# Performance work log

Hardware: AMD Instinct MI355X
Metric: run time of the kernel (lower is better)

## Reference

```python
import jax, jax.numpy as jnp
import numpy as np

C_Z = 128
N_HEADS = 4
HEAD_DIM = 32
TOTAL = N_HEADS * HEAD_DIM
B, N = 1, 256


def setup_inputs() -> dict:
    key = jax.random.key(0)
    ks = jax.random.split(key, 10)
    s = lambda k, sh: jax.random.normal(k, sh, dtype=jnp.float32) * 0.02
    return {
        "pair_representation": jax.random.normal(ks[0], (B, N, N, C_Z), dtype=jnp.float32),
        "ln_gamma": jnp.ones((C_Z,), jnp.float32),
        "ln_beta": jnp.zeros((C_Z,), jnp.float32),
        "Wq": s(ks[1], (C_Z, TOTAL)),
        "Wk": s(ks[2], (C_Z, TOTAL)),
        "Wv": s(ks[3], (C_Z, TOTAL)),
        "Wb": s(ks[4], (C_Z, N_HEADS)),
        "Wg": s(ks[5], (C_Z, TOTAL)),
        "bg": jnp.zeros((TOTAL,), jnp.float32),
        "Wo": s(ks[6], (TOTAL, C_Z)),
        "bo": jnp.zeros((C_Z,), jnp.float32),
    }


def reference(pair_representation, ln_gamma, ln_beta, Wq, Wk, Wv, Wb, Wg, bg, Wo, bo):
    x = pair_representation
    # LayerNorm over c_z
    mu = jnp.mean(x, axis=-1, keepdims=True)
    var = jnp.mean((x - mu) ** 2, axis=-1, keepdims=True)
    x = (x - mu) * jax.lax.rsqrt(var + 1e-5) * ln_gamma + ln_beta

    b, n, _, _ = x.shape
    split = lambda t: t.reshape(b, n, n, N_HEADS, HEAD_DIM)
    Q = split(x @ Wq)  # [b,i,j,h,d]
    K = split(x @ Wk)
    V = split(x @ Wv)
    G = jax.nn.sigmoid(split(x @ Wg + bg))
    Bias = x @ Wb  # [b,j,k,h]

    scores = jnp.einsum("bijhd,bikhd->bijkh", Q, K) / np.float32(np.sqrt(HEAD_DIM))
    scores = scores + Bias[:, None]  # broadcast over i
    attn = jax.nn.softmax(scores, axis=3)  # over k
    vals = jnp.einsum("bijkh,bikhd->bijhd", attn, V)
    vals = (G * vals).reshape(b, n, n, TOTAL)
    return vals @ Wo + bo
```

## Files before the change

### kernel.cpp

```cpp
#include <hip/hip_runtime.h>
#include <hip/hip_bf16.h>


#define QSCALE 0.17677669529663687f

typedef __attribute__((ext_vector_type(8))) short bf16x8;
typedef __attribute__((ext_vector_type(4))) short bf16x4;
typedef __attribute__((ext_vector_type(4))) float f32x4;

#define MFMA32(a, b, c) __builtin_amdgcn_mfma_f32_16x16x32_bf16((a), (b), (c), 0, 0, 0)

__device__ __forceinline__ f32x4 mfma16_asm(bf16x4 a, bf16x4 b, f32x4 c) {
    f32x4 d;
    asm volatile("v_mfma_f32_16x16x16_bf16 %0, %1, %2, %3"
                 : "=v"(d) : "v"(a), "v"(b), "v"(c));
    return d;
}

#if !defined(__HIP_DEVICE_COMPILE__)
#define MFMA16(a, b, c) (c)
#elif __has_builtin(__builtin_amdgcn_mfma_f32_16x16x16bf16_1k)
#define MFMA16(a, b, c) __builtin_amdgcn_mfma_f32_16x16x16bf16_1k((a), (b), (c), 0, 0, 0)
#else
#define MFMA16(a, b, c) mfma16_asm((a), (b), (c))
#endif

__device__ __forceinline__ ushort f2bf(float f) {
    uint32_t u = __builtin_bit_cast(uint32_t, f);
    uint32_t r = (u + 0x7FFFu + ((u >> 16) & 1u)) >> 16;
    return (ushort)r;
}
__device__ __forceinline__ uint pk2(float a, float b) {
    union { __hip_bfloat162 h; uint u; } cv;
    cv.h = __float22bfloat162_rn(make_float2(a, b));
    return cv.u;
}

__global__ __launch_bounds__(256) void prep_bias_kernel(
    const float* __restrict__ Wq, const float* __restrict__ Wk, const float* __restrict__ Wv,
    const float* __restrict__ Wg, const float* __restrict__ Wo, const float* __restrict__ Wb,
    const float* __restrict__ x, const float* __restrict__ gamma, const float* __restrict__ beta,
    ushort* __restrict__ Wfrag, ushort* __restrict__ WoFrag,
    ushort* __restrict__ xn, float* __restrict__ BbF)
{
    __shared__ float WbS[512];
    __shared__ float gS[128];
    __shared__ float bS[128];

    if (blockIdx.x < 320) {
        int idx = blockIdx.x * 256 + threadIdx.x;
        if (idx < 65536) {
            int j = idx & 7, lane = (idx >> 3) & 63, ks = (idx >> 9) & 3, ct = idx >> 11;
            int n = ct * 16 + (lane & 15);
            int k = ks * 32 + (lane >> 4) * 8 + j;
            float v;
            if (n < 128)      v = Wq[k * 128 + n] * QSCALE;
            else if (n < 256) v = Wk[k * 128 + (n - 128)];
            else if (n < 384) v = Wv[k * 128 + (n - 256)];
            else              v = Wg[k * 128 + (n - 384)];
            Wfrag[idx] = f2bf(v);
        } else {
            int idx2 = idx - 65536;
            int j = idx2 & 7, lane = (idx2 >> 3) & 63, ks = (idx2 >> 9) & 3, ct = idx2 >> 11;
            int n = ct * 16 + (lane & 15);
            int k = ks * 32 + (lane >> 4) * 8 + j;
            WoFrag[idx2] = f2bf(Wo[k * 128 + n]);
        }
        return;
    }

    const int t = threadIdx.x;
    if (t < 128)      { *(f32x4*)&WbS[t * 4] = *(const f32x4*)(Wb + t * 4); }
    else if (t < 160) { int c = (t - 128) * 4; *(f32x4*)&gS[c] = *(const f32x4*)(gamma + c); }
    else if (t < 192) { int c = (t - 160) * 4; *(f32x4*)&bS[c] = *(const f32x4*)(beta + c); }
    __syncthreads();

    const int wave = t >> 6, lane = t & 63, m = lane & 15, quad = lane >> 4;
    const int p = (blockIdx.x - 320) * 64 + wave * 16 + m;

    const float* rp0 = x + (size_t)p * 128;
    f32x4 xa[4][2];
    float sum = 0.f, ssq = 0.f;
#pragma unroll
    for (int ks = 0; ks < 4; ++ks) {
        xa[ks][0] = *(const f32x4*)(rp0 + ks * 32 + quad * 8);
        xa[ks][1] = *(const f32x4*)(rp0 + ks * 32 + quad * 8 + 4);
#pragma unroll
        for (int q4 = 0; q4 < 2; ++q4) {
            f32x4 v = xa[ks][q4];
            sum += v[0] + v[1] + v[2] + v[3];
            ssq += v[0]*v[0] + v[1]*v[1] + v[2]*v[2] + v[3]*v[3];
        }
    }
    sum += __shfl_xor(sum, 16); ssq += __shfl_xor(ssq, 16);
    sum += __shfl_xor(sum, 32); ssq += __shfl_xor(ssq, 32);
    const float mu   = sum * (1.f / 128.f);
    const float rstd = rsqrtf(ssq * (1.f / 128.f) - mu * mu + 1e-5f);

    float b0 = 0.f, b1 = 0.f, b2 = 0.f, b3 = 0.f;
#pragma unroll
    for (int ks = 0; ks < 4; ++ks) {
        uint4 pkd;
        uint pw[4];
#pragma unroll
        for (int q4 = 0; q4 < 2; ++q4) {
            const int c = ks * 32 + quad * 8 + q4 * 4;
            f32x4 v = xa[ks][q4];
            float n0 = (v[0] - mu) * rstd * gS[c + 0] + bS[c + 0];
            float n1 = (v[1] - mu) * rstd * gS[c + 1] + bS[c + 1];
            float n2 = (v[2] - mu) * rstd * gS[c + 2] + bS[c + 2];
            float n3 = (v[3] - mu) * rstd * gS[c + 3] + bS[c + 3];
            pw[q4 * 2]     = pk2(n0, n1);
            pw[q4 * 2 + 1] = pk2(n2, n3);
            f32x4 w0 = *(const f32x4*)&WbS[(c + 0) * 4];
            f32x4 w1 = *(const f32x4*)&WbS[(c + 1) * 4];
            f32x4 w2 = *(const f32x4*)&WbS[(c + 2) * 4];
            f32x4 w3 = *(const f32x4*)&WbS[(c + 3) * 4];
            b0 += n0*w0[0] + n1*w1[0] + n2*w2[0] + n3*w3[0];
            b1 += n0*w0[1] + n1*w1[1] + n2*w2[1] + n3*w3[1];
            b2 += n0*w0[2] + n1*w1[2] + n2*w2[2] + n3*w3[2];
            b3 += n0*w0[3] + n1*w1[3] + n2*w2[3] + n3*w3[3];
        }
        pkd.x = pw[0]; pkd.y = pw[1]; pkd.z = pw[2]; pkd.w = pw[3];
        *(uint4*)(xn + (size_t)p * 128 + ks * 32 + quad * 8) = pkd;
    }
    b0 += __shfl_xor(b0, 16); b1 += __shfl_xor(b1, 16); b2 += __shfl_xor(b2, 16); b3 += __shfl_xor(b3, 16);
    b0 += __shfl_xor(b0, 32); b1 += __shfl_xor(b1, 32); b2 += __shfl_xor(b2, 32); b3 += __shfl_xor(b3, 32);

    if (quad == 0) {
        const int row = p >> 8, col = p & 255;
        float bb[4] = {b0, b1, b2, b3};
#pragma unroll
        for (int r = 0; r < 4; ++r) {
            int addr = (((r * 16 + (row >> 4)) * 16 + (col >> 4)) * 64 +
                        ((col & 15) >> 2) * 16 + (row & 15)) * 4 + (col & 3);
            BbF[addr] = bb[r];
        }
    }
}

__global__ __launch_bounds__(256, 4) void fused_kernel(
    const ushort* __restrict__ xn, const ushort* __restrict__ Wfrag,
    const float* __restrict__ bg, const float* __restrict__ BbF,
    ushort* __restrict__ gvals)
{
    __shared__ __align__(16) ushort SM[18688];
    ushort* QK = SM;
    ushort* VT = SM + 10240;

    const int t = threadIdx.x;
    const int w = t >> 6, lane = t & 63, m = lane & 15, quad = lane >> 4;
    const int i = blockIdx.x >> 2, h = blockIdx.x & 3;
    const ushort* xb = xn + ((size_t)i << 15);

    {
        const ushort* Wm = Wfrag + (0 + h * 2) * 2048;
        bf16x8 wfr[2][4];
#pragma unroll
        for (int ctl = 0; ctl < 2; ++ctl)
#pragma unroll
            for (int ks = 0; ks < 4; ++ks)
                wfr[ctl][ks] = *(const bf16x8*)(Wm + ctl * 2048 + ks * 512 + lane * 8);
#pragma unroll
        for (int grp = 0; grp < 4; ++grp) {
            const int j = w * 64 + grp * 16 + m;
            bf16x8 xg[4];
            const ushort* xp = xb + (size_t)j * 128 + quad * 8;
#pragma unroll
            for (int ks = 0; ks < 4; ++ks) xg[ks] = *(const bf16x8*)(xp + ks * 32);
#pragma unroll
            for (int ctl = 0; ctl < 2; ++ctl) {
                f32x4 acc = (f32x4){0.f, 0.f, 0.f, 0.f};
#pragma unroll
                for (int ks = 0; ks < 4; ++ks) acc = MFMA32(wfr[ctl][ks], xg[ks], acc);
                uint2 u; u.x = pk2(acc[0], acc[1]); u.y = pk2(acc[2], acc[3]);
                *(uint2*)(QK + j * 40 + ctl * 16 + quad * 4) = u;
            }
        }
    }
    bf16x8 qf[4];
#pragma unroll
    for (int jt = 0; jt < 4; ++jt)
        qf[jt] = *(const bf16x8*)(QK + (w * 64 + jt * 16 + m) * 40 + quad * 8);
    asm volatile("" ::: "memory");

    {
        const ushort* Wm = Wfrag + (8 + h * 2) * 2048;
        bf16x8 wfr[2][4];
#pragma unroll
        for (int ctl = 0; ctl < 2; ++ctl)
#pragma unroll
            for (int ks = 0; ks < 4; ++ks)
                wfr[ctl][ks] = *(const bf16x8*)(Wm + ctl * 2048 + ks * 512 + lane * 8);
#pragma unroll
        for (int grp = 0; grp < 4; ++grp) {
            const int k = w * 64 + grp * 16 + m;
            bf16x8 xg[4];
            const ushort* xp = xb + (size_t)k * 128 + quad * 8;
#pragma unroll
            for (int ks = 0; ks < 4; ++ks) xg[ks] = *(const bf16x8*)(xp + ks * 32);
#pragma unroll
            for (int ctl = 0; ctl < 2; ++ctl) {
                f32x4 acc = (f32x4){0.f, 0.f, 0.f, 0.f};
#pragma unroll
                for (int ks = 0; ks < 4; ++ks) acc = MFMA32(wfr[ctl][ks], xg[ks], acc);
                uint2 u; u.x = pk2(acc[0], acc[1]); u.y = pk2(acc[2], acc[3]);
                *(uint2*)(QK + k * 40 + ctl * 16 + quad * 4) = u;
            }
        }
    }
    asm volatile("" ::: "memory");

    {
        const ushort* Wm = Wfrag + (16 + h * 2) * 2048;
        bf16x8 wfr[2][4];
#pragma unroll
        for (int ctl = 0; ctl < 2; ++ctl)
#pragma unroll
            for (int ks = 0; ks < 4; ++ks)
                wfr[ctl][ks] = *(const bf16x8*)(Wm + ctl * 2048 + ks * 512 + lane * 8);
#pragma unroll
        for (int grp = 0; grp < 4; ++grp) {
            const int k = w * 64 + grp * 16 + m;
            bf16x8 xg[4];
            const ushort* xp = xb + (size_t)k * 128 + quad * 8;
#pragma unroll
            for (int ks = 0; ks < 4; ++ks) xg[ks] = *(const bf16x8*)(xp + ks * 32);
#pragma unroll
            for (int ctl = 0; ctl < 2; ++ctl) {
                f32x4 acc = (f32x4){0.f, 0.f, 0.f, 0.f};
#pragma unroll
                for (int ks = 0; ks < 4; ++ks) acc = MFMA32(wfr[ctl][ks], xg[ks], acc);
#pragma unroll
                for (int r = 0; r < 4; ++r)
                    VT[(ctl * 16 + quad * 4 + r) * 264 + k] = f2bf(acc[r]);
            }
        }
    }
    __syncthreads();

    f32x4 O[4][2];
    float lsum[4];
#pragma unroll
    for (int jt = 0; jt < 4; ++jt) {
        O[jt][0] = (f32x4){0.f, 0.f, 0.f, 0.f};
        O[jt][1] = (f32x4){0.f, 0.f, 0.f, 0.f};
        lsum[jt] = 0.f;
    }
    const float* bb = BbF + ((size_t)(h * 16 + w * 4) << 12) + (lane << 2);

    for (int kh = 0; kh < 16; ++kh) {
        bf16x8 kf = *(const bf16x8*)(QK + (kh * 16 + m) * 40 + quad * 8);
        bf16x4 vf[2];
#pragma unroll
        for (int dt = 0; dt < 2; ++dt) {
            uint2 vv = *(const uint2*)(VT + (dt * 16 + m) * 264 + kh * 16 + quad * 4);
            vf[dt] = __builtin_bit_cast(bf16x4, vv);
        }
#pragma unroll
        for (int jt = 0; jt < 4; ++jt) {
            f32x4 S = *(const f32x4*)(bb + (jt << 12) + (kh << 8));
            S = MFMA32(kf, qf[jt], S);
            float p0 = __expf(S[0]), p1 = __expf(S[1]);
            float p2 = __expf(S[2]), p3 = __expf(S[3]);
            lsum[jt] += p0 + p1 + p2 + p3;
            uint2 pu; pu.x = pk2(p0, p1); pu.y = pk2(p2, p3);
            bf16x4 pf = __builtin_bit_cast(bf16x4, pu);
#pragma unroll
            for (int dt = 0; dt < 2; ++dt)
                O[jt][dt] = MFMA16(vf[dt], pf, O[jt][dt]);
        }
    }

#pragma unroll
    for (int jt = 0; jt < 4; ++jt) {
        float s = lsum[jt];
        s += __shfl_xor(s, 16);
        s += __shfl_xor(s, 32);
        lsum[jt] = 1.f / s;
    }

    {
        const ushort* Wm = Wfrag + (24 + h * 2) * 2048;
        bf16x8 wfr[2][4];
        f32x4 bg4[2];
#pragma unroll
        for (int ctl = 0; ctl < 2; ++ctl) {
#pragma unroll
            for (int ks = 0; ks < 4; ++ks)
                wfr[ctl][ks] = *(const bf16x8*)(Wm + ctl * 2048 + ks * 512 + lane * 8);
            bg4[ctl] = *(const f32x4*)(bg + h * 32 + ctl * 16 + quad * 4);
        }
#pragma unroll
        for (int grp = 0; grp < 4; ++grp) {
            const int j = w * 64 + grp * 16 + m;
            const float rl = lsum[grp];
            bf16x8 xg[4];
            const ushort* xp = xb + (size_t)j * 128 + quad * 8;
#pragma unroll
            for (int ks = 0; ks < 4; ++ks) xg[ks] = *(const bf16x8*)(xp + ks * 32);
#pragma unroll
            for (int ctl = 0; ctl < 2; ++ctl) {
                f32x4 acc = (f32x4){0.f, 0.f, 0.f, 0.f};
#pragma unroll
                for (int ks = 0; ks < 4; ++ks) acc = MFMA32(wfr[ctl][ks], xg[ks], acc);
                float g0 = 1.f / (1.f + __expf(-(acc[0] + bg4[ctl][0])));
                float g1 = 1.f / (1.f + __expf(-(acc[1] + bg4[ctl][1])));
                float g2 = 1.f / (1.f + __expf(-(acc[2] + bg4[ctl][2])));
                float g3 = 1.f / (1.f + __expf(-(acc[3] + bg4[ctl][3])));
                float v0 = O[grp][ctl][0] * rl * g0;
                float v1 = O[grp][ctl][1] * rl * g1;
                float v2 = O[grp][ctl][2] * rl * g2;
                float v3 = O[grp][ctl][3] * rl * g3;
                uint2 u; u.x = pk2(v0, v1); u.y = pk2(v2, v3);
                *(uint2*)(gvals + (size_t)(i * 256 + j) * 128 + h * 32 + ctl * 16 + quad * 4) = u;
            }
        }
    }
}

__global__ __launch_bounds__(256) void oproj_kernel(
    const ushort* __restrict__ gvals, const ushort* __restrict__ WoFrag,
    const float* __restrict__ bo, float* __restrict__ out)
{
    __shared__ ushort Bs[8 * 2048];
    const int t = threadIdx.x;
    const int wave = t >> 6, lane = t & 63, m = lane & 15, quad = lane >> 4;
    const int p0 = blockIdx.x * 64;
    {
        const uint4* src = (const uint4*)WoFrag;
        uint4* dst = (uint4*)Bs;
#pragma unroll
        for (int r = 0; r < 8; ++r) dst[r * 256 + t] = src[r * 256 + t];
    }
    bf16x8 gf[4];
    const int p = p0 + wave * 16 + m;
#pragma unroll
    for (int ks = 0; ks < 4; ++ks)
        gf[ks] = *(const bf16x8*)(gvals + (size_t)p * 128 + ks * 32 + quad * 8);
    __syncthreads();

#pragma unroll
    for (int ct = 0; ct < 8; ++ct) {
        f32x4 acc = (f32x4){0.f, 0.f, 0.f, 0.f};
#pragma unroll
        for (int ks = 0; ks < 4; ++ks) {
            bf16x8 wfr = ((const bf16x8*)Bs)[(ct * 4 + ks) * 64 + lane];
            acc = MFMA32(wfr, gf[ks], acc);
        }
        const int c0 = ct * 16 + quad * 4;
        f32x4 bov = *(const f32x4*)(bo + c0);
        float4 v = make_float4(acc[0] + bov[0], acc[1] + bov[1],
                               acc[2] + bov[2], acc[3] + bov[3]);
        *(float4*)(&out[(size_t)p * 128 + c0]) = v;
    }
}

extern "C" void kernel_launch(void* const* d_in, const int* in_sizes, int n_in,
                              void* d_out, int out_size, void* d_ws, size_t ws_size,
                              hipStream_t stream) {
    const float* x     = (const float*)d_in[0];
    const float* gamma = (const float*)d_in[1];
    const float* beta  = (const float*)d_in[2];
    const float* Wq    = (const float*)d_in[3];
    const float* Wk    = (const float*)d_in[4];
    const float* Wv    = (const float*)d_in[5];
    const float* Wb    = (const float*)d_in[6];
    const float* Wg    = (const float*)d_in[7];
    const float* bg    = (const float*)d_in[8];
    const float* Wo    = (const float*)d_in[9];
    const float* bo    = (const float*)d_in[10];

    ushort* ws      = (ushort*)d_ws;
    ushort* Wfrag   = ws;
    ushort* WoFragp = ws + 65536;
    ushort* xn      = ws + 81920;
    ushort* gvals   = ws + 81920 + 8388608;
    float*  BbF     = (float*)(ws + 81920 + 2 * 8388608);

    prep_bias_kernel<<<1344, 256, 0, stream>>>(Wq, Wk, Wv, Wg, Wo, Wb,
                                               x, gamma, beta,
                                               Wfrag, WoFragp, xn, BbF);
    fused_kernel<<<1024, 256, 0, stream>>>(xn, Wfrag, bg, BbF, gvals);
    oproj_kernel<<<1024, 256, 0, stream>>>(gvals, WoFragp, bo, (float*)d_out);
}
```

Before: 172.6 us.

## Fuse output projection into attention kernel with one block per row

Merges the separate output-projection kernel into the attention kernel. Each 512-thread block now covers one row i across all four heads, so the gated values are staged in shared memory and multiplied by Wo in place, with no global round trip. The pair bias is also pre-exponentiated in the prep kernel, turning the in-loop bias add into a multiply of exp(S). Shared memory layouts are XOR-swizzled to avoid bank conflicts. In exchange the kernel uses 128KB of dynamic shared memory with one block per CU and only 256 blocks, which cuts occupancy and the parallelism available to hide latency.

Result: faster. 162.5 us (-5.9%).

```diff
diff --git a/kernel.cpp b/kernel.cpp
--- a/kernel.cpp
+++ b/kernel.cpp
@@ -41,7 +41,7 @@
     const float* __restrict__ Wg, const float* __restrict__ Wo, const float* __restrict__ Wb,
     const float* __restrict__ x, const float* __restrict__ gamma, const float* __restrict__ beta,
     ushort* __restrict__ Wfrag, ushort* __restrict__ WoFrag,
-    ushort* __restrict__ xn, float* __restrict__ BbF)
+    ushort* __restrict__ xn, float* __restrict__ EbF)
 {
     __shared__ float WbS[512];
     __shared__ float gS[128];
@@ -134,27 +134,32 @@
         for (int r = 0; r < 4; ++r) {
             int addr = (((r * 16 + (row >> 4)) * 16 + (col >> 4)) * 64 +
                         ((col & 15) >> 2) * 16 + (row & 15)) * 4 + (col & 3);
-            BbF[addr] = bb[r];
-        }
-    }
-}
-
-__global__ __launch_bounds__(256, 4) void fused_kernel(
+            EbF[addr] = __expf(bb[r]);
+        }
+    }
+}
+
+__global__ __launch_bounds__(512, 1) void fused_kernel(
     const ushort* __restrict__ xn, const ushort* __restrict__ Wfrag,
-    const float* __restrict__ bg, const float* __restrict__ BbF,
-    ushort* __restrict__ gvals)
+    const float* __restrict__ bg, const float* __restrict__ EbF,
+    const ushort* __restrict__ WoFrag, const float* __restrict__ bo,
+    float* __restrict__ out)
 {
-    __shared__ __align__(16) ushort SM[18688];
-    ushort* QK = SM;
-    ushort* VT = SM + 10240;
+    extern __shared__ __align__(16) ushort SM[];
+    ushort* KL = SM;
+    ushort* VT = SM + 32768;
+
+    const f32x4 ZERO4 = {0.f, 0.f, 0.f, 0.f};
 
     const int t = threadIdx.x;
     const int w = t >> 6, lane = t & 63, m = lane & 15, quad = lane >> 4;
-    const int i = blockIdx.x >> 2, h = blockIdx.x & 3;
+    const int i = blockIdx.x;
+    const int h = w >> 1, half = w & 1;
+    const int jbase = half * 128;
     const ushort* xb = xn + ((size_t)i << 15);
 
     {
-        const ushort* Wm = Wfrag + (0 + h * 2) * 2048;
+        const ushort* Wm = Wfrag + (h * 2) * 2048;
         bf16x8 wfr[2][4];
 #pragma unroll
         for (int ctl = 0; ctl < 2; ++ctl)
@@ -162,26 +167,31 @@
             for (int ks = 0; ks < 4; ++ks)
                 wfr[ctl][ks] = *(const bf16x8*)(Wm + ctl * 2048 + ks * 512 + lane * 8);
 #pragma unroll
-        for (int grp = 0; grp < 4; ++grp) {
-            const int j = w * 64 + grp * 16 + m;
+        for (int grp = 0; grp < 8; ++grp) {
+            const int jloc = grp * 16 + m;
             bf16x8 xg[4];
-            const ushort* xp = xb + (size_t)j * 128 + quad * 8;
+            const ushort* xp = xb + (size_t)(jbase + jloc) * 128 + quad * 8;
 #pragma unroll
             for (int ks = 0; ks < 4; ++ks) xg[ks] = *(const bf16x8*)(xp + ks * 32);
 #pragma unroll
             for (int ctl = 0; ctl < 2; ++ctl) {
-                f32x4 acc = (f32x4){0.f, 0.f, 0.f, 0.f};
+                f32x4 acc = ZERO4;
 #pragma unroll
                 for (int ks = 0; ks < 4; ++ks) acc = MFMA32(wfr[ctl][ks], xg[ks], acc);
+                const int c = ctl * 16 + quad * 4;
+                const int idx = (w * 4096 + jloc * 32 + c) ^ ((jloc & 3) << 3);
                 uint2 u; u.x = pk2(acc[0], acc[1]); u.y = pk2(acc[2], acc[3]);
-                *(uint2*)(QK + j * 40 + ctl * 16 + quad * 4) = u;
+                *(uint2*)(KL + idx) = u;
             }
         }
     }
-    bf16x8 qf[4];
-#pragma unroll
-    for (int jt = 0; jt < 4; ++jt)
-        qf[jt] = *(const bf16x8*)(QK + (w * 64 + jt * 16 + m) * 40 + quad * 8);
+    bf16x8 qf[8];
+#pragma unroll
+    for (int jt = 0; jt < 8; ++jt) {
+        const int jloc = jt * 16 + m;
+        const int idx = (w * 4096 + jloc * 32 + quad * 8) ^ ((jloc & 3) << 3);
+        qf[jt] = *(const bf16x8*)(KL + idx);
+    }
     asm volatile("" ::: "memory");
 
     {
@@ -193,23 +203,24 @@
             for (int ks = 0; ks < 4; ++ks)
                 wfr[ctl][ks] = *(const bf16x8*)(Wm + ctl * 2048 + ks * 512 + lane * 8);
 #pragma unroll
-        for (int grp = 0; grp < 4; ++grp) {
-            const int k = w * 64 + grp * 16 + m;
+        for (int grp = 0; grp < 8; ++grp) {
+            const int k = jbase + grp * 16 + m;
             bf16x8 xg[4];
             const ushort* xp = xb + (size_t)k * 128 + quad * 8;
 #pragma unroll
             for (int ks = 0; ks < 4; ++ks) xg[ks] = *(const bf16x8*)(xp + ks * 32);
 #pragma unroll
             for (int ctl = 0; ctl < 2; ++ctl) {
-                f32x4 acc = (f32x4){0.f, 0.f, 0.f, 0.f};
+                f32x4 acc = ZERO4;
 #pragma unroll
                 for (int ks = 0; ks < 4; ++ks) acc = MFMA32(wfr[ctl][ks], xg[ks], acc);
+                const int d0 = ctl * 16 + quad * 4;
+                const int idx = (h * 8192 + (k >> 1) * 64 + (k & 1) * 32 + d0) ^ (((k >> 1) & 7) << 3);
                 uint2 u; u.x = pk2(acc[0], acc[1]); u.y = pk2(acc[2], acc[3]);
-                *(uint2*)(QK + k * 40 + ctl * 16 + quad * 4) = u;
+                *(uint2*)(KL + idx) = u;
             }
         }
     }
-    asm volatile("" ::: "memory");
 
     {
         const ushort* Wm = Wfrag + (16 + h * 2) * 2048;
@@ -220,49 +231,61 @@
             for (int ks = 0; ks < 4; ++ks)
                 wfr[ctl][ks] = *(const bf16x8*)(Wm + ctl * 2048 + ks * 512 + lane * 8);
 #pragma unroll
-        for (int grp = 0; grp < 4; ++grp) {
-            const int k = w * 64 + grp * 16 + m;
+        for (int grp = 0; grp < 8; ++grp) {
+            const int k = jbase + grp * 16 + m;
             bf16x8 xg[4];
             const ushort* xp = xb + (size_t)k * 128 + quad * 8;
 #pragma unroll
             for (int ks = 0; ks < 4; ++ks) xg[ks] = *(const bf16x8*)(xp + ks * 32);
 #pragma unroll
             for (int ctl = 0; ctl < 2; ++ctl) {
-                f32x4 acc = (f32x4){0.f, 0.f, 0.f, 0.f};
+                f32x4 acc = ZERO4;
 #pragma unroll
                 for (int ks = 0; ks < 4; ++ks) acc = MFMA32(wfr[ctl][ks], xg[ks], acc);
 #pragma unroll
-                for (int r = 0; r < 4; ++r)
-                    VT[(ctl * 16 + quad * 4 + r) * 264 + k] = f2bf(acc[r]);
+                for (int r = 0; r < 4; ++r) {
+                    const int d = ctl * 16 + quad * 4 + r;
+                    const int idx = ((h * 32 + d) * 256 + k) ^ ((d & 7) << 3);
+                    VT[idx] = f2bf(acc[r]);
+                }
             }
         }
     }
     __syncthreads();
 
-    f32x4 O[4][2];
-    float lsum[4];
-#pragma unroll
-    for (int jt = 0; jt < 4; ++jt) {
-        O[jt][0] = (f32x4){0.f, 0.f, 0.f, 0.f};
-        O[jt][1] = (f32x4){0.f, 0.f, 0.f, 0.f};
+    f32x4 O[8][2];
+    float lsum[8];
+#pragma unroll
+    for (int jt = 0; jt < 8; ++jt) {
+        O[jt][0] = ZERO4;
+        O[jt][1] = ZERO4;
         lsum[jt] = 0.f;
     }
-    const float* bb = BbF + ((size_t)(h * 16 + w * 4) << 12) + (lane << 2);
+    const float* ebB = EbF + ((size_t)(h * 16 + half * 8) << 12) + (lane << 2);
 
     for (int kh = 0; kh < 16; ++kh) {
-        bf16x8 kf = *(const bf16x8*)(QK + (kh * 16 + m) * 40 + quad * 8);
+        f32x4 eb[8];
+#pragma unroll
+        for (int jt = 0; jt < 8; ++jt)
+            eb[jt] = *(const f32x4*)(ebB + (jt << 12) + (kh << 8));
+        const int k = kh * 16 + m;
+        const int kidx = (h * 8192 + (k >> 1) * 64 + (k & 1) * 32 + quad * 8) ^ (((k >> 1) & 7) << 3);
+        bf16x8 kf = *(const bf16x8*)(KL + kidx);
         bf16x4 vf[2];
 #pragma unroll
         for (int dt = 0; dt < 2; ++dt) {
-            uint2 vv = *(const uint2*)(VT + (dt * 16 + m) * 264 + kh * 16 + quad * 4);
+            const int d = dt * 16 + m;
+            const int vidx = ((h * 32 + d) * 256 + kh * 16 + quad * 4) ^ ((d & 7) << 3);
+            uint2 vv = *(const uint2*)(VT + vidx);
             vf[dt] = __builtin_bit_cast(bf16x4, vv);
         }
 #pragma unroll
-        for (int jt = 0; jt < 4; ++jt) {
-            f32x4 S = *(const f32x4*)(bb + (jt << 12) + (kh << 8));
-            S = MFMA32(kf, qf[jt], S);
-            float p0 = __expf(S[0]), p1 = __expf(S[1]);
-            float p2 = __expf(S[2]), p3 = __expf(S[3]);
+        for (int jt = 0; jt < 8; ++jt) {
+            f32x4 S = MFMA32(kf, qf[jt], ZERO4);
+            float p0 = __expf(S[0]) * eb[jt][0];
+            float p1 = __expf(S[1]) * eb[jt][1];
+            float p2 = __expf(S[2]) * eb[jt][2];
+            float p3 = __expf(S[3]) * eb[jt][3];
             lsum[jt] += p0 + p1 + p2 + p3;
             uint2 pu; pu.x = pk2(p0, p1); pu.y = pk2(p2, p3);
             bf16x4 pf = __builtin_bit_cast(bf16x4, pu);
@@ -273,13 +296,14 @@
     }
 
 #pragma unroll
-    for (int jt = 0; jt < 4; ++jt) {
+    for (int jt = 0; jt < 8; ++jt) {
         float s = lsum[jt];
         s += __shfl_xor(s, 16);
         s += __shfl_xor(s, 32);
         lsum[jt] = 1.f / s;
     }
 
+    uint2 gva[8][2];
     {
         const ushort* Wm = Wfrag + (24 + h * 2) * 2048;
         bf16x8 wfr[2][4];
@@ -292,16 +316,15 @@
             bg4[ctl] = *(const f32x4*)(bg + h * 32 + ctl * 16 + quad * 4);
         }
 #pragma unroll
-        for (int grp = 0; grp < 4; ++grp) {
-            const int j = w * 64 + grp * 16 + m;
+        for (int grp = 0; grp < 8; ++grp) {
             const float rl = lsum[grp];
             bf16x8 xg[4];
-            const ushort* xp = xb + (size_t)j * 128 + quad * 8;
+            const ushort* xp = xb + (size_t)(jbase + grp * 16 + m) * 128 + quad * 8;
 #pragma unroll
             for (int ks = 0; ks < 4; ++ks) xg[ks] = *(const bf16x8*)(xp + ks * 32);
 #pragma unroll
             for (int ctl = 0; ctl < 2; ++ctl) {
-                f32x4 acc = (f32x4){0.f, 0.f, 0.f, 0.f};
+                f32x4 acc = ZERO4;
 #pragma unroll
                 for (int ks = 0; ks < 4; ++ks) acc = MFMA32(wfr[ctl][ks], xg[ks], acc);
                 float g0 = 1.f / (1.f + __expf(-(acc[0] + bg4[ctl][0])));
@@ -312,47 +335,53 @@
                 float v1 = O[grp][ctl][1] * rl * g1;
                 float v2 = O[grp][ctl][2] * rl * g2;
                 float v3 = O[grp][ctl][3] * rl * g3;
-                uint2 u; u.x = pk2(v0, v1); u.y = pk2(v2, v3);
-                *(uint2*)(gvals + (size_t)(i * 256 + j) * 128 + h * 32 + ctl * 16 + quad * 4) = u;
+                gva[grp][ctl].x = pk2(v0, v1);
+                gva[grp][ctl].y = pk2(v2, v3);
             }
         }
     }
-}
-
-__global__ __launch_bounds__(256) void oproj_kernel(
-    const ushort* __restrict__ gvals, const ushort* __restrict__ WoFrag,
-    const float* __restrict__ bo, float* __restrict__ out)
-{
-    __shared__ ushort Bs[8 * 2048];
-    const int t = threadIdx.x;
-    const int wave = t >> 6, lane = t & 63, m = lane & 15, quad = lane >> 4;
-    const int p0 = blockIdx.x * 64;
-    {
-        const uint4* src = (const uint4*)WoFrag;
-        uint4* dst = (uint4*)Bs;
-#pragma unroll
-        for (int r = 0; r < 8; ++r) dst[r * 256 + t] = src[r * 256 + t];
-    }
-    bf16x8 gf[4];
-    const int p = p0 + wave * 16 + m;
-#pragma unroll
-    for (int ks = 0; ks < 4; ++ks)
-        gf[ks] = *(const bf16x8*)(gvals + (size_t)p * 128 + ks * 32 + quad * 8);
     __syncthreads();
 
 #pragma unroll
+    for (int grp = 0; grp < 8; ++grp) {
+        const int j = jbase + grp * 16 + m;
+#pragma unroll
+        for (int ctl = 0; ctl < 2; ++ctl) {
+            const int c0 = h * 32 + ctl * 16 + quad * 4;
+            const int idx = (j * 128 + c0) ^ ((j & 7) << 3);
+            *(uint2*)(KL + idx) = gva[grp][ctl];
+        }
+    }
+    __syncthreads();
+
+    bf16x8 gf[2][4];
+#pragma unroll
+    for (int grp = 0; grp < 2; ++grp) {
+        const int pl = w * 32 + grp * 16 + m;
+#pragma unroll
+        for (int ks = 0; ks < 4; ++ks) {
+            const int idx = (pl * 128 + ks * 32 + quad * 8) ^ ((pl & 7) << 3);
+            gf[grp][ks] = *(const bf16x8*)(KL + idx);
+        }
+    }
+#pragma unroll
     for (int ct = 0; ct < 8; ++ct) {
-        f32x4 acc = (f32x4){0.f, 0.f, 0.f, 0.f};
-#pragma unroll
-        for (int ks = 0; ks < 4; ++ks) {
-            bf16x8 wfr = ((const bf16x8*)Bs)[(ct * 4 + ks) * 64 + lane];
-            acc = MFMA32(wfr, gf[ks], acc);
-        }
+        bf16x8 wfr[4];
+#pragma unroll
+        for (int ks = 0; ks < 4; ++ks)
+            wfr[ks] = *(const bf16x8*)(WoFrag + (ct * 4 + ks) * 512 + lane * 8);
         const int c0 = ct * 16 + quad * 4;
         f32x4 bov = *(const f32x4*)(bo + c0);
-        float4 v = make_float4(acc[0] + bov[0], acc[1] + bov[1],
-                               acc[2] + bov[2], acc[3] + bov[3]);
-        *(float4*)(&out[(size_t)p * 128 + c0]) = v;
+#pragma unroll
+        for (int grp = 0; grp < 2; ++grp) {
+            f32x4 acc = ZERO4;
+#pragma unroll
+            for (int ks = 0; ks < 4; ++ks) acc = MFMA32(wfr[ks], gf[grp][ks], acc);
+            const int p = i * 256 + w * 32 + grp * 16 + m;
+            float4 v = make_float4(acc[0] + bov[0], acc[1] + bov[1],
+                                   acc[2] + bov[2], acc[3] + bov[3]);
+            *(float4*)(out + (size_t)p * 128 + c0) = v;
+        }
     }
 }
 
@@ -375,12 +404,18 @@
     ushort* Wfrag   = ws;
     ushort* WoFragp = ws + 65536;
     ushort* xn      = ws + 81920;
-    ushort* gvals   = ws + 81920 + 8388608;
-    float*  BbF     = (float*)(ws + 81920 + 2 * 8388608);
+    float*  EbF     = (float*)(ws + 81920 + 8388608);
+
+    static bool attr_set = false;
+    if (!attr_set) {
+        (void)hipFuncSetAttribute((const void*)fused_kernel,
+                                  hipFuncAttributeMaxDynamicSharedMemorySize, 131072);
+        attr_set = true;
+    }
 
     prep_bias_kernel<<<1344, 256, 0, stream>>>(Wq, Wk, Wv, Wg, Wo, Wb,
                                                x, gamma, beta,
-                                               Wfrag, WoFragp, xn, BbF);
-    fused_kernel<<<1024, 256, 0, stream>>>(xn, Wfrag, bg, BbF, gvals);
-    oproj_kernel<<<1024, 256, 0, stream>>>(gvals, WoFragp, bo, (float*)d_out);
-}
+                                               Wfrag, WoFragp, xn, EbF);
+    fused_kernel<<<256, 512, 131072, stream>>>(xn, Wfrag, bg, EbF,
+                                               WoFragp, bo, (float*)d_out);
+}
```
